# Optimization experiments

Hardware: AMD Instinct MI355X
Metric: run time of the kernel (lower is better)

## Reference

```python
import jax, jax.numpy as jnp
import numpy as np

BETA = 0.25  # commitment_beta


def _mlp(x, Ws, bs):
    # hidden layers with ReLU, final linear layer without activation
    h = x
    for W, b in zip(Ws[:-1], bs[:-1]):
        h = jax.nn.relu(h @ W + b)
    return h @ Ws[-1] + bs[-1]


def _vq(r, cb):
    # r: [B, D], cb: [K, D]
    # squared L2 distances via expansion: ||r||^2 - 2 r.cb^T + ||cb||^2
    d = (jnp.sum(r * r, axis=1, keepdims=True)
         - 2.0 * (r @ cb.T)
         + jnp.sum(cb * cb, axis=1))  # [B, K]
    idx = jnp.argmin(d, axis=1)  # [B]
    e = cb[idx]  # [B, D]
    sg = jax.lax.stop_gradient
    # per-sample codebook + commitment loss
    loss = (jnp.mean((sg(r) - e) ** 2, axis=1)
            + BETA * jnp.mean((r - sg(e)) ** 2, axis=1))  # [B]
    # straight-through estimator
    z_q = r + sg(e - r)
    return z_q, loss, idx


def setup_inputs() -> dict:
    key = jax.random.key(0)
    ks = jax.random.split(key, 16)
    B, D_IN, H1, H2, D_LAT, K = 16384, 2048, 1024, 512, 256, 1024

    def lin(k, fan_in, fan_out):
        s = 1.0 / np.sqrt(fan_in)
        return jax.random.uniform(k, (fan_in, fan_out), jnp.float32, -s, s)

    return {
        "x": jax.random.normal(ks[0], (B, D_IN), jnp.float32),
        "enc_W1": lin(ks[1], D_IN, H1), "enc_b1": jnp.zeros((H1,), jnp.float32),
        "enc_W2": lin(ks[2], H1, H2), "enc_b2": jnp.zeros((H2,), jnp.float32),
        "enc_W3": lin(ks[3], H2, D_LAT), "enc_b3": jnp.zeros((D_LAT,), jnp.float32),
        "ln_g": jnp.ones((D_LAT,), jnp.float32),
        "ln_b": jnp.zeros((D_LAT,), jnp.float32),
        "cb0": jax.random.normal(ks[4], (K, D_LAT), jnp.float32) * 0.02,
        "cb1": jax.random.normal(ks[5], (K, D_LAT), jnp.float32) * 0.02,
        "cb2": jax.random.normal(ks[6], (K, D_LAT), jnp.float32) * 0.02,
        "dec_W1": lin(ks[7], D_LAT, H2), "dec_b1": jnp.zeros((H2,), jnp.float32),
        "dec_W2": lin(ks[8], H2, H1), "dec_b2": jnp.zeros((H1,), jnp.float32),
        "dec_W3": lin(ks[9], H1, D_IN), "dec_b3": jnp.zeros((D_IN,), jnp.float32),
    }


def reference(x, enc_W1, enc_b1, enc_W2, enc_b2, enc_W3, enc_b3,
              ln_g, ln_b, cb0, cb1, cb2,
              dec_W1, dec_b1, dec_W2, dec_b2, dec_W3, dec_b3):
    z = _mlp(x, [enc_W1, enc_W2, enc_W3], [enc_b1, enc_b2, enc_b3])
    # LayerNorm over latent dim
    mu = jnp.mean(z, axis=-1, keepdims=True)
    var = jnp.var(z, axis=-1, keepdims=True)
    z = (z - mu) * jax.lax.rsqrt(var + 1e-5) * ln_g + ln_b

    sg = jax.lax.stop_gradient
    residual = z
    z_q_total = jnp.zeros_like(z)
    losses, indices = [], []
    for cb in (cb0, cb1, cb2):
        z_q, vloss, idx = _vq(residual, cb)
        residual = residual - sg(z_q)
        z_q_total = z_q_total + z_q
        losses.append(vloss)
        indices.append(idx)

    x_hat = _mlp(z_q_total, [dec_W1, dec_W2, dec_W3], [dec_b1, dec_b2, dec_b3])
    recon_loss = jnp.mean((x_hat - x) ** 2, axis=1)  # [B]
    loss = jnp.sum(jnp.stack(losses, axis=1), axis=1) + recon_loss  # [B]
    idx_out = jnp.stack(indices, axis=1)  # [B, 3]
    return x_hat, loss, idx_out
```

## Files before the change

kernel.cpp:

```cpp
#include <hip/hip_runtime.h>
#include <stdint.h>

typedef __bf16 bf16x8 __attribute__((ext_vector_type(8)));
typedef _Float16 f16x8 __attribute__((ext_vector_type(8)));
typedef float f32x4 __attribute__((ext_vector_type(4)));

#define BETA 0.25f

__device__ __forceinline__ unsigned short f2bf(float f) {
    __bf16 h = (__bf16)f;
    return __builtin_bit_cast(unsigned short, h);
}

__device__ __forceinline__ unsigned short f2h(float f) {
    _Float16 h = (_Float16)f;
    return __builtin_bit_cast(unsigned short, h);
}

__device__ __forceinline__ void split8(const float* a, uint4& vh, uint4& vl) {
    unsigned h[8], l[8];
#pragma unroll
    for (int j = 0; j < 8; ++j) {
        _Float16 hi = (_Float16)a[j];
        float hf = (float)hi;
        _Float16 lo = (_Float16)((a[j] - hf) * 2048.0f);
        h[j] = (unsigned)__builtin_bit_cast(unsigned short, hi);
        l[j] = (unsigned)__builtin_bit_cast(unsigned short, lo);
    }
    vh.x = h[0] | (h[1] << 16); vh.y = h[2] | (h[3] << 16);
    vh.z = h[4] | (h[5] << 16); vh.w = h[6] | (h[7] << 16);
    vl.x = l[0] | (l[1] << 16); vl.y = l[2] | (l[3] << 16);
    vl.z = l[4] | (l[5] << 16); vl.w = l[6] | (l[7] << 16);
}

__global__ __launch_bounds__(256) void wsplit_t(
    const float* __restrict__ W, unsigned short* __restrict__ WTh,
    unsigned short* __restrict__ WTl, int K, int N)
{
    __shared__ float tile[32][33];
    const int t = threadIdx.x;
    const int n0 = blockIdx.x * 32, k0 = blockIdx.y * 32;
    const int rr = t >> 3, c4 = (t & 7) * 4;
    float4 w = *(const float4*)(W + (size_t)(k0 + rr) * N + n0 + c4);
    tile[rr][c4 + 0] = w.x; tile[rr][c4 + 1] = w.y;
    tile[rr][c4 + 2] = w.z; tile[rr][c4 + 3] = w.w;
    __syncthreads();
    float v[4] = {tile[c4 + 0][rr], tile[c4 + 1][rr],
                  tile[c4 + 2][rr], tile[c4 + 3][rr]};
    unsigned short hh[4], ll[4];
#pragma unroll
    for (int j = 0; j < 4; ++j) {
        float s = v[j] * 32.0f;
        _Float16 hi = (_Float16)s;
        float hf = (float)hi;
        hh[j] = __builtin_bit_cast(unsigned short, hi);
        ll[j] = f2h((s - hf) * 2048.0f);
    }
    ushort4 oh, ol;
    oh.x = hh[0]; oh.y = hh[1]; oh.z = hh[2]; oh.w = hh[3];
    ol.x = ll[0]; ol.y = ll[1]; ol.z = ll[2]; ol.w = ll[3];
    *(ushort4*)(WTh + (size_t)(n0 + rr) * K + k0 + c4) = oh;
    *(ushort4*)(WTl + (size_t)(n0 + rr) * K + k0 + c4) = ol;
}

template <bool AF32, bool RELU, bool OUTSPLIT>
__global__ __launch_bounds__(256, 2) void gemm_f16x2(
    const float* __restrict__ Af,
    const unsigned short* __restrict__ Ah, const unsigned short* __restrict__ Al,
    const unsigned short* __restrict__ WTh, const unsigned short* __restrict__ WTl,
    const float* __restrict__ bias,
    void* __restrict__ Oh, unsigned short* __restrict__ Ol,
    int M, int N, int K)
{
    __shared__ unsigned short Ash[2][128][36];
    __shared__ unsigned short Asl[2][128][36];
    __shared__ unsigned short Bsh[2][128][36];
    __shared__ unsigned short Bsl[2][128][36];

    const int t = threadIdx.x;
    const int m0 = blockIdx.y * 128, n0 = blockIdx.x * 128;
    const int wave = t >> 6, lane = t & 63;
    const int wm = wave & 1, wn = wave >> 1;
    const int l15 = lane & 15, kq = lane >> 4;

    f32x4 ach[4][4] = {};
    f32x4 acl[4][4] = {};

    const int sr = t >> 1, skc = (t & 1) * 16;

    float af[16];
    uint4 vah, vah2, val, val2;
    uint4 vbh, vbh2, vbl, vbl2;

    auto LOAD = [&](int kb) {
        if (AF32) {
            const float* ap = Af + (size_t)(m0 + sr) * K + kb + skc;
            *(float4*)&af[0]  = *(const float4*)(ap);
            *(float4*)&af[4]  = *(const float4*)(ap + 4);
            *(float4*)&af[8]  = *(const float4*)(ap + 8);
            *(float4*)&af[12] = *(const float4*)(ap + 12);
        } else {
            const unsigned short* aph = Ah + (size_t)(m0 + sr) * K + kb + skc;
            const unsigned short* apl = Al + (size_t)(m0 + sr) * K + kb + skc;
            vah  = *(const uint4*)(aph);
            vah2 = *(const uint4*)(aph + 8);
            val  = *(const uint4*)(apl);
            val2 = *(const uint4*)(apl + 8);
        }
        const unsigned short* bph = WTh + (size_t)(n0 + sr) * K + kb + skc;
        const unsigned short* bpl = WTl + (size_t)(n0 + sr) * K + kb + skc;
        vbh  = *(const uint4*)(bph);
        vbh2 = *(const uint4*)(bph + 8);
        vbl  = *(const uint4*)(bpl);
        vbl2 = *(const uint4*)(bpl + 8);
    };

    auto STORE = [&](int buf) {
        uint4 wah, wah2, wal, wal2;
        if (AF32) {
            split8(&af[0], wah, wal);
            split8(&af[8], wah2, wal2);
        } else {
            wah = vah; wah2 = vah2; wal = val; wal2 = val2;
        }
        *(uint4*)&Ash[buf][sr][skc]     = wah;
        *(uint4*)&Ash[buf][sr][skc + 8] = wah2;
        *(uint4*)&Asl[buf][sr][skc]     = wal;
        *(uint4*)&Asl[buf][sr][skc + 8] = wal2;
        *(uint4*)&Bsh[buf][sr][skc]     = vbh;
        *(uint4*)&Bsh[buf][sr][skc + 8] = vbh2;
        *(uint4*)&Bsl[buf][sr][skc]     = vbl;
        *(uint4*)&Bsl[buf][sr][skc + 8] = vbl2;
    };

    const int nt = K >> 5;
    LOAD(0);
    STORE(0);
    int cur = 0;
    for (int ti = 0; ti < nt; ++ti) {
        __syncthreads();
        if (ti + 1 < nt) LOAD((ti + 1) << 5);

        f16x8 bh[4], bl[4];
#pragma unroll
        for (int bn = 0; bn < 4; ++bn) {
            bh[bn] = *(const f16x8*)&Bsh[cur][wn * 64 + bn * 16 + l15][kq * 8];
            bl[bn] = *(const f16x8*)&Bsl[cur][wn * 64 + bn * 16 + l15][kq * 8];
        }
#pragma unroll
        for (int am = 0; am < 4; ++am) {
            f16x8 ah_ = *(const f16x8*)&Ash[cur][wm * 64 + am * 16 + l15][kq * 8];
            f16x8 al_ = *(const f16x8*)&Asl[cur][wm * 64 + am * 16 + l15][kq * 8];
#pragma unroll
            for (int bn = 0; bn < 4; ++bn) {
                ach[am][bn] = __builtin_amdgcn_mfma_f32_16x16x32_f16(ah_, bh[bn], ach[am][bn], 0, 0, 0);
                acl[am][bn] = __builtin_amdgcn_mfma_f32_16x16x32_f16(ah_, bl[bn], acl[am][bn], 0, 0, 0);
                acl[am][bn] = __builtin_amdgcn_mfma_f32_16x16x32_f16(al_, bh[bn], acl[am][bn], 0, 0, 0);
            }
        }
        if (ti + 1 < nt) STORE(cur ^ 1);
        cur ^= 1;
    }

#pragma unroll
    for (int am = 0; am < 4; ++am)
#pragma unroll
        for (int bn = 0; bn < 4; ++bn)
#pragma unroll
            for (int r = 0; r < 4; ++r) {
                int row = m0 + wm * 64 + am * 16 + kq * 4 + r;
                int col = n0 + wn * 64 + bn * 16 + l15;
                float v = (ach[am][bn][r] + acl[am][bn][r] * (1.0f / 2048.0f))
                          * (1.0f / 32.0f) + bias[col];
                if (RELU) v = fmaxf(v, 0.0f);
                if (OUTSPLIT) {
                    _Float16 hi = (_Float16)v;
                    float hf = (float)hi;
                    ((unsigned short*)Oh)[(size_t)row * N + col] =
                        __builtin_bit_cast(unsigned short, hi);
                    Ol[(size_t)row * N + col] = f2h((v - hf) * 2048.0f);
                } else {
                    ((float*)Oh)[(size_t)row * N + col] = v;
                }
            }
}

template <bool RELU, bool OUTF32>
__global__ __launch_bounds__(256) void gemm_bt128(
    const unsigned short* __restrict__ A, const unsigned short* __restrict__ WT,
    const float* __restrict__ bias, void* __restrict__ Ov,
    int M, int N, int K)
{
    __shared__ unsigned short As[2][128][36];
    __shared__ unsigned short Bs[2][128][36];

    const int t = threadIdx.x;
    const int m0 = blockIdx.y * 128, n0 = blockIdx.x * 128;
    const int wave = t >> 6, lane = t & 63;
    const int wm = wave & 1, wn = wave >> 1;
    const int l15 = lane & 15, kq = lane >> 4;

    f32x4 acc[4][4] = {};

    const int sr = t >> 1, skc = (t & 1) * 16;

    uint4 va, va2, vb, vb2;
    auto LOAD = [&](int kb) {
        const unsigned short* ap = A + (size_t)(m0 + sr) * K + kb + skc;
        const unsigned short* bp = WT + (size_t)(n0 + sr) * K + kb + skc;
        va  = *(const uint4*)(ap);
        va2 = *(const uint4*)(ap + 8);
        vb  = *(const uint4*)(bp);
        vb2 = *(const uint4*)(bp + 8);
    };
    auto STORE = [&](int buf) {
        *(uint4*)&As[buf][sr][skc]     = va;
        *(uint4*)&As[buf][sr][skc + 8] = va2;
        *(uint4*)&Bs[buf][sr][skc]     = vb;
        *(uint4*)&Bs[buf][sr][skc + 8] = vb2;
    };

    const int nt = K >> 5;
    LOAD(0);
    STORE(0);
    int cur = 0;
    for (int ti = 0; ti < nt; ++ti) {
        __syncthreads();
        if (ti + 1 < nt) LOAD((ti + 1) << 5);

        bf16x8 bfr[4];
#pragma unroll
        for (int bn = 0; bn < 4; ++bn)
            bfr[bn] = *(const bf16x8*)&Bs[cur][wn * 64 + bn * 16 + l15][kq * 8];
#pragma unroll
        for (int am = 0; am < 4; ++am) {
            bf16x8 af = *(const bf16x8*)&As[cur][wm * 64 + am * 16 + l15][kq * 8];
#pragma unroll
            for (int bn = 0; bn < 4; ++bn)
                acc[am][bn] = __builtin_amdgcn_mfma_f32_16x16x32_bf16(af, bfr[bn], acc[am][bn], 0, 0, 0);
        }
        if (ti + 1 < nt) STORE(cur ^ 1);
        cur ^= 1;
    }

#pragma unroll
    for (int am = 0; am < 4; ++am)
#pragma unroll
        for (int bn = 0; bn < 4; ++bn)
#pragma unroll
            for (int r = 0; r < 4; ++r) {
                int row = m0 + wm * 64 + am * 16 + kq * 4 + r;
                int col = n0 + wn * 64 + bn * 16 + l15;
                float v = acc[am][bn][r] + bias[col];
                if (RELU) v = fmaxf(v, 0.0f);
                if (OUTF32)
                    ((float*)Ov)[(size_t)row * N + col] = v;
                else
                    ((unsigned short*)Ov)[(size_t)row * N + col] = f2bf(v);
            }
}

__global__ __launch_bounds__(256) void wtrans(
    const float* __restrict__ W, unsigned short* __restrict__ WT, int K, int N)
{
    __shared__ unsigned short tile[32][33];
    const int t = threadIdx.x;
    const int n0 = blockIdx.x * 32, k0 = blockIdx.y * 32;
    const int r = t >> 3, c4 = (t & 7) * 4;
    float4 w = *(const float4*)(W + (size_t)(k0 + r) * N + n0 + c4);
    tile[r][c4 + 0] = f2bf(w.x);
    tile[r][c4 + 1] = f2bf(w.y);
    tile[r][c4 + 2] = f2bf(w.z);
    tile[r][c4 + 3] = f2bf(w.w);
    __syncthreads();
    ushort4 o;
    o.x = tile[c4 + 0][r]; o.y = tile[c4 + 1][r];
    o.z = tile[c4 + 2][r]; o.w = tile[c4 + 3][r];
    *(ushort4*)(WT + (size_t)(n0 + r) * K + k0 + c4) = o;
}

__global__ __launch_bounds__(256) void ln_kernel(
    const float* __restrict__ Z, const float* __restrict__ g,
    const float* __restrict__ b, float* __restrict__ R)
{
    int row = blockIdx.x * 4 + (threadIdx.x >> 6);
    int lane = threadIdx.x & 63;
    float4 v = *(const float4*)(Z + (size_t)row * 256 + lane * 4);
    float s = v.x + v.y + v.z + v.w;
#pragma unroll
    for (int o = 32; o; o >>= 1) s += __shfl_xor(s, o);
    float mu = s * (1.0f / 256.0f);
    float4 d = {v.x - mu, v.y - mu, v.z - mu, v.w - mu};
    float q = d.x * d.x + d.y * d.y + d.z * d.z + d.w * d.w;
#pragma unroll
    for (int o = 32; o; o >>= 1) q += __shfl_xor(q, o);
    float var = q * (1.0f / 256.0f);
    float rs = 1.0f / sqrtf(var + 1e-5f);
    int c0 = lane * 4;
    float4 gg = *(const float4*)(g + c0);
    float4 bb = *(const float4*)(b + c0);
    float4 o4;
    o4.x = d.x * rs * gg.x + bb.x;
    o4.y = d.y * rs * gg.y + bb.y;
    o4.z = d.z * rs * gg.z + bb.z;
    o4.w = d.w * rs * gg.w + bb.w;
    *(float4*)(R + (size_t)row * 256 + c0) = o4;
}

__global__ __launch_bounds__(256) void cninit3(
    const float* __restrict__ CB0, const float* __restrict__ CB1,
    const float* __restrict__ CB2, float* __restrict__ cn,
    unsigned long long* __restrict__ amin)
{
    int b = blockIdx.x;
    int s = b >> 6, lb = b & 63;
    int g = lb * 256 + threadIdx.x;
    amin[(size_t)s * 16384 + g] = 0xFFFFFFFFFFFFFFFFULL;
    if (g < 1024) {
        const float* CB = (s == 0) ? CB0 : (s == 1) ? CB1 : CB2;
        const float* p = CB + (size_t)g * 256;
        float sum = 0.f;
        for (int d = 0; d < 256; ++d) sum = fmaf(p[d], p[d], sum);
        cn[s * 1024 + g] = sum;
    }
}

__global__ __launch_bounds__(256) void rn_kernel(
    const float* __restrict__ R, float* __restrict__ rn)
{
    __shared__ float rs[16][260];
    const int t = threadIdx.x, r0 = blockIdx.x * 16;
    {
        int row = t >> 4, j = t & 15;
#pragma unroll
        for (int q = 0; q < 4; ++q) {
            int col = j * 16 + q * 4;
            *(float4*)&rs[row][col] = *(const float4*)(R + (size_t)(r0 + row) * 256 + col);
        }
    }
    __syncthreads();
    if (t < 16) {
        float s = 0.f;
        for (int d = 0; d < 256; ++d) s = fmaf(rs[t][d], rs[t][d], s);
        rn[r0 + t] = s;
    }
}

__global__ __launch_bounds__(256) void vq_dist(
    const float* __restrict__ Rbuf, const float* __restrict__ CB,
    const float* __restrict__ rn, const float* __restrict__ cn,
    unsigned long long* __restrict__ amin)
{
    __shared__ char smem[33792];
    float (*As)[16][132] = (float (*)[16][132])smem;
    float (*Bs)[16][132] = (float (*)[16][132])(smem + 16896);
    unsigned long long (*red)[17] = (unsigned long long (*)[17])smem;

    const int t = threadIdx.x;
    const int m0 = blockIdx.y * 128, n0 = blockIdx.x * 128;
    const int tx = t & 15, ty = t >> 4;
    float c[8][8] = {};

    const int sr = t >> 1, skc = (t & 1) * 8;

    float4 a0, a1, b0, b1;
    auto LOAD = [&](int kb) {
        const float* ap = Rbuf + (size_t)(m0 + sr) * 256 + kb + skc;
        a0 = *(const float4*)(ap);
        a1 = *(const float4*)(ap + 4);
        const float* bp = CB + (size_t)(n0 + sr) * 256 + kb + skc;
        b0 = *(const float4*)(bp);
        b1 = *(const float4*)(bp + 4);
    };
    auto STORE = [&](int buf) {
        As[buf][skc + 0][sr] = a0.x; As[buf][skc + 1][sr] = a0.y;
        As[buf][skc + 2][sr] = a0.z; As[buf][skc + 3][sr] = a0.w;
        As[buf][skc + 4][sr] = a1.x; As[buf][skc + 5][sr] = a1.y;
        As[buf][skc + 6][sr] = a1.z; As[buf][skc + 7][sr] = a1.w;
        Bs[buf][skc + 0][sr] = b0.x; Bs[buf][skc + 1][sr] = b0.y;
        Bs[buf][skc + 2][sr] = b0.z; Bs[buf][skc + 3][sr] = b0.w;
        Bs[buf][skc + 4][sr] = b1.x; Bs[buf][skc + 5][sr] = b1.y;
        Bs[buf][skc + 6][sr] = b1.z; Bs[buf][skc + 7][sr] = b1.w;
    };

    LOAD(0);
    STORE(0);
    int cur = 0;
    for (int ti = 0; ti < 16; ++ti) {
        __syncthreads();
        if (ti + 1 < 16) LOAD((ti + 1) * 16);

#pragma unroll
        for (int k = 0; k < 16; ++k) {
            float a[8], b[8];
            *(float4*)&a[0] = *(const float4*)&As[cur][k][ty * 8];
            *(float4*)&a[4] = *(const float4*)&As[cur][k][ty * 8 + 4];
            *(float4*)&b[0] = *(const float4*)&Bs[cur][k][tx * 4];
            *(float4*)&b[4] = *(const float4*)&Bs[cur][k][64 + tx * 4];
#pragma unroll
            for (int i = 0; i < 8; ++i)
#pragma unroll
                for (int j = 0; j < 8; ++j)
                    c[i][j] = fmaf(a[i], b[j], c[i][j]);
        }
        if (ti + 1 < 16) STORE(cur ^ 1);
        cur ^= 1;
    }

    float rnv[8], cnv[8];
    *(float4*)&rnv[0] = *(const float4*)(rn + m0 + ty * 8);
    *(float4*)&rnv[4] = *(const float4*)(rn + m0 + ty * 8 + 4);
    *(float4*)&cnv[0] = *(const float4*)(cn + n0 + tx * 4);
    *(float4*)&cnv[4] = *(const float4*)(cn + n0 + 64 + tx * 4);

    __syncthreads();

#pragma unroll
    for (int i = 0; i < 8; ++i) {
        unsigned long long best = 0xFFFFFFFFFFFFFFFFULL;
#pragma unroll
        for (int j = 0; j < 8; ++j) {
            float dist = (rnv[i] - 2.0f * c[i][j]) + cnv[j];
            int col = n0 + (j < 4 ? tx * 4 + j : 64 + tx * 4 + (j - 4));
            unsigned long long p =
                ((unsigned long long)__builtin_bit_cast(unsigned int, dist) << 32) |
                (unsigned int)col;
            if (p < best) best = p;
        }
        red[ty * 8 + i][tx] = best;
    }
    __syncthreads();
    if (t < 128) {
        unsigned long long b = red[t][0];
#pragma unroll
        for (int j = 1; j < 16; ++j) {
            unsigned long long v = red[t][j];
            if (v < b) b = v;
        }
        atomicMin(amin + m0 + t, b);
    }
}

__global__ __launch_bounds__(256) void vq_update(
    float* __restrict__ Rbuf, float* __restrict__ ZQ, float* __restrict__ lossf,
    const float* __restrict__ CB, const unsigned long long* __restrict__ amin,
    float* __restrict__ idx_out, unsigned short* __restrict__ ZQB, int stage)
{
    __shared__ float lred[16][17];
    const int t = threadIdx.x, r0 = blockIdx.x * 16;
    const int row = r0 + (t >> 4), c16 = (t & 15) * 16;
    unsigned int idx = (unsigned int)(amin[row] & 0xffffffffu);
    const float* e = CB + (size_t)idx * 256 + c16;
    float* rp = Rbuf + (size_t)row * 256 + c16;
    float* zp = ZQ + (size_t)row * 256 + c16;
    float part = 0.f;
#pragma unroll
    for (int q = 0; q < 4; ++q) {
        float4 ev = *(const float4*)(e + q * 4);
        float4 rv = *(const float4*)(rp + q * 4);
        float4 dv = {rv.x - ev.x, rv.y - ev.y, rv.z - ev.z, rv.w - ev.w};
        *(float4*)(rp + q * 4) = dv;
        if (stage == 0) {
            *(float4*)(zp + q * 4) = ev;
        } else if (stage == 1) {
            float4 zv = *(const float4*)(zp + q * 4);
            zv.x += ev.x; zv.y += ev.y; zv.z += ev.z; zv.w += ev.w;
            *(float4*)(zp + q * 4) = zv;
        } else {
            float4 zv = *(const float4*)(zp + q * 4);
            zv.x += ev.x; zv.y += ev.y; zv.z += ev.z; zv.w += ev.w;
            ushort4 zb;
            zb.x = f2bf(zv.x); zb.y = f2bf(zv.y);
            zb.z = f2bf(zv.z); zb.w = f2bf(zv.w);
            *(ushort4*)(ZQB + (size_t)row * 256 + c16 + q * 4) = zb;
        }
        part = fmaf(dv.x, dv.x, part);
        part = fmaf(dv.y, dv.y, part);
        part = fmaf(dv.z, dv.z, part);
        part = fmaf(dv.w, dv.w, part);
    }
    lred[t >> 4][t & 15] = part;
    __syncthreads();
    if (t < 16) {
        float s = 0.f;
        for (int j = 0; j < 16; ++j) s += lred[t][j];
        float m = s * (1.0f / 256.0f);
        float l = m + BETA * m;
        int gr = r0 + t;
        if (stage == 0) lossf[gr] = l;
        else            lossf[gr] += l;
        idx_out[(size_t)gr * 3 + stage] =
            (float)(unsigned int)(amin[gr] & 0xffffffffu);
    }
}

__global__ __launch_bounds__(256) void recon_kernel(
    const float* __restrict__ XH, const float* __restrict__ X,
    const float* __restrict__ LOSS_IN, float* __restrict__ LOSS_OUT)
{
    __shared__ float wsum[4];
    int row = blockIdx.x, t = threadIdx.x;
    float4 h0 = *(const float4*)(XH + (size_t)row * 2048 + t * 8);
    float4 h1 = *(const float4*)(XH + (size_t)row * 2048 + t * 8 + 4);
    float4 x0 = *(const float4*)(X + (size_t)row * 2048 + t * 8);
    float4 x1 = *(const float4*)(X + (size_t)row * 2048 + t * 8 + 4);
    float h[8] = {h0.x, h0.y, h0.z, h0.w, h1.x, h1.y, h1.z, h1.w};
    float xv[8] = {x0.x, x0.y, x0.z, x0.w, x1.x, x1.y, x1.z, x1.w};
    float s = 0.f;
#pragma unroll
    for (int j = 0; j < 8; ++j) {
        float d = h[j] - xv[j];
        s = fmaf(d, d, s);
    }
#pragma unroll
    for (int o = 32; o; o >>= 1) s += __shfl_xor(s, o);
    if ((t & 63) == 0) wsum[t >> 6] = s;
    __syncthreads();
    if (t == 0) {
        float tot = wsum[0] + wsum[1] + wsum[2] + wsum[3];
        LOSS_OUT[row] = LOSS_IN[row] + tot * (1.0f / 2048.0f);
    }
}

extern "C" void kernel_launch(void* const* d_in, const int* in_sizes, int n_in,
                              void* d_out, int out_size, void* d_ws, size_t ws_size,
                              hipStream_t stream)
{
    const float* x      = (const float*)d_in[0];
    const float* enc_W1 = (const float*)d_in[1];
    const float* enc_b1 = (const float*)d_in[2];
    const float* enc_W2 = (const float*)d_in[3];
    const float* enc_b2 = (const float*)d_in[4];
    const float* enc_W3 = (const float*)d_in[5];
    const float* enc_b3 = (const float*)d_in[6];
    const float* ln_g   = (const float*)d_in[7];
    const float* ln_b   = (const float*)d_in[8];
    const float* cb0    = (const float*)d_in[9];
    const float* cb1    = (const float*)d_in[10];
    const float* cb2    = (const float*)d_in[11];
    const float* dec_W1 = (const float*)d_in[12];
    const float* dec_b1 = (const float*)d_in[13];
    const float* dec_W2 = (const float*)d_in[14];
    const float* dec_b2 = (const float*)d_in[15];
    const float* dec_W3 = (const float*)d_in[16];
    const float* dec_b3 = (const float*)d_in[17];

    const int B = 16384, D_IN = 2048, H1 = 1024, H2 = 512, D_LAT = 256;

    char* ws = (char*)d_ws;
    unsigned short* h1h = (unsigned short*)(ws);
    unsigned short* h1l = (unsigned short*)(ws + (32u << 20));
    unsigned short* h2h = (unsigned short*)(ws + (64u << 20));
    unsigned short* h2l = (unsigned short*)(ws + (80u << 20));
    float* z     = (float*)(ws + (96u << 20));
    float* r     = (float*)(ws + (112u << 20));
    float* zq    = (float*)(ws + (96u << 20));
    unsigned short* w1th = (unsigned short*)(ws + (96u << 20));
    unsigned short* w1tl = (unsigned short*)(ws + (100u << 20));
    unsigned short* w2th = (unsigned short*)(ws + (104u << 20));
    unsigned short* w2tl = (unsigned short*)(ws + (105u << 20));
    unsigned short* w3th = (unsigned short*)(ws + (112u << 20));
    unsigned short* w3tl = (unsigned short*)(ws + (113u << 20));
    unsigned short* d1  = (unsigned short*)(ws);
    unsigned short* d2  = (unsigned short*)(ws + (16u << 20));
    unsigned short* wt3 = (unsigned short*)(ws + (48u << 20));
    unsigned short* wt2 = (unsigned short*)(ws + (52u << 20));
    float* lossf = (float*)(ws + (64u << 20));
    float* cn3   = (float*)(ws + (65u << 20));
    unsigned long long* amin3 = (unsigned long long*)(ws + (66u << 20));
    float* rnb   = (float*)(ws + (67u << 20));
    unsigned short* zqb = (unsigned short*)(ws + (68u << 20));
    unsigned short* wt1 = (unsigned short*)(ws + (76u << 20));

    float* xhat     = (float*)d_out;
    float* loss_out = xhat + (size_t)B * D_IN;
    float* idx_out  = loss_out + B;

    wsplit_t<<<dim3(H1 / 32, D_IN / 32), 256, 0, stream>>>(enc_W1, w1th, w1tl, D_IN, H1);
    wsplit_t<<<dim3(H2 / 32, H1 / 32), 256, 0, stream>>>(enc_W2, w2th, w2tl, H1, H2);
    wsplit_t<<<dim3(D_LAT / 32, H2 / 32), 256, 0, stream>>>(enc_W3, w3th, w3tl, H2, D_LAT);

    gemm_f16x2<true, true, true><<<dim3(H1 / 128, B / 128), 256, 0, stream>>>(
        x, nullptr, nullptr, w1th, w1tl, enc_b1, h1h, h1l, B, H1, D_IN);
    gemm_f16x2<false, true, true><<<dim3(H2 / 128, B / 128), 256, 0, stream>>>(
        nullptr, h1h, h1l, w2th, w2tl, enc_b2, h2h, h2l, B, H2, H1);
    wtrans<<<dim3(H1 / 32, H2 / 32), 256, 0, stream>>>(dec_W2, wt2, H2, H1);
    wtrans<<<dim3(D_IN / 32, H1 / 32), 256, 0, stream>>>(dec_W3, wt3, H1, D_IN);
    gemm_f16x2<false, false, false><<<dim3(D_LAT / 128, B / 128), 256, 0, stream>>>(
        nullptr, h2h, h2l, w3th, w3tl, enc_b3, z, nullptr, B, D_LAT, H2);
    ln_kernel<<<B / 4, 256, 0, stream>>>(z, ln_g, ln_b, r);

    cninit3<<<192, 256, 0, stream>>>(cb0, cb1, cb2, cn3, amin3);
    wtrans<<<dim3(H2 / 32, D_LAT / 32), 256, 0, stream>>>(dec_W1, wt1, D_LAT, H2);

    const float* cbs[3] = {cb0, cb1, cb2};
    for (int s = 0; s < 3; ++s) {
        rn_kernel<<<B / 16, 256, 0, stream>>>(r, rnb);
        vq_dist<<<dim3(1024 / 128, B / 128), 256, 0, stream>>>(
            r, cbs[s], rnb, cn3 + s * 1024, amin3 + (size_t)s * 16384);
        vq_update<<<B / 16, 256, 0, stream>>>(
            r, zq, lossf, cbs[s], amin3 + (size_t)s * 16384, idx_out, zqb, s);
    }

    gemm_bt128<true, false><<<dim3(H2 / 128, B / 128), 256, 0, stream>>>(
        zqb, wt1, dec_b1, d1, B, H2, D_LAT);
    gemm_bt128<true, false><<<dim3(H1 / 128, B / 128), 256, 0, stream>>>(
        d1, wt2, dec_b2, d2, B, H1, H2);
    gemm_bt128<false, true><<<dim3(D_IN / 128, B / 128), 256, 0, stream>>>(
        d2, wt3, dec_b3, xhat, B, D_IN, H1);
    recon_kernel<<<B, 256, 0, stream>>>(xhat, x, lossf, loss_out);
}
```

Measured before the change: 1.330 ms.

## Replace double-buffered LDS pipeline in vq_dist with single-buffer two-barrier loop

The codebook distance GEMM kernel drops its register-prefetch double buffering and goes back to one LDS buffer, with two barriers per k-tile. The reduction scratch becomes its own shared array instead of aliasing the tile buffers. This lowers register pressure and may raise occupancy, but global loads are no longer overlapped with the FMA work of the previous tile. Shared memory use goes up because the reduction array is now separate.

```diff
diff --git a/kernel.cpp b/kernel.cpp
--- a/kernel.cpp
+++ b/kernel.cpp
@@ -351,10 +351,9 @@
     const float* __restrict__ rn, const float* __restrict__ cn,
     unsigned long long* __restrict__ amin)
 {
-    __shared__ char smem[33792];
-    float (*As)[16][132] = (float (*)[16][132])smem;
-    float (*Bs)[16][132] = (float (*)[16][132])(smem + 16896);
-    unsigned long long (*red)[17] = (unsigned long long (*)[17])smem;
+    __shared__ float As[16][132];
+    __shared__ float Bs[16][132];
+    __shared__ unsigned long long red[128][17];
 
     const int t = threadIdx.x;
     const int m0 = blockIdx.y * 128, n0 = blockIdx.x * 128;
@@ -363,48 +362,38 @@
 
     const int sr = t >> 1, skc = (t & 1) * 8;
 
-    float4 a0, a1, b0, b1;
-    auto LOAD = [&](int kb) {
+    for (int kb = 0; kb < 256; kb += 16) {
         const float* ap = Rbuf + (size_t)(m0 + sr) * 256 + kb + skc;
-        a0 = *(const float4*)(ap);
-        a1 = *(const float4*)(ap + 4);
+        float4 a0 = *(const float4*)(ap);
+        float4 a1 = *(const float4*)(ap + 4);
         const float* bp = CB + (size_t)(n0 + sr) * 256 + kb + skc;
-        b0 = *(const float4*)(bp);
-        b1 = *(const float4*)(bp + 4);
-    };
-    auto STORE = [&](int buf) {
-        As[buf][skc + 0][sr] = a0.x; As[buf][skc + 1][sr] = a0.y;
-        As[buf][skc + 2][sr] = a0.z; As[buf][skc + 3][sr] = a0.w;
-        As[buf][skc + 4][sr] = a1.x; As[buf][skc + 5][sr] = a1.y;
-        As[buf][skc + 6][sr] = a1.z; As[buf][skc + 7][sr] = a1.w;
-        Bs[buf][skc + 0][sr] = b0.x; Bs[buf][skc + 1][sr] = b0.y;
-        Bs[buf][skc + 2][sr] = b0.z; Bs[buf][skc + 3][sr] = b0.w;
-        Bs[buf][skc + 4][sr] = b1.x; Bs[buf][skc + 5][sr] = b1.y;
-        Bs[buf][skc + 6][sr] = b1.z; Bs[buf][skc + 7][sr] = b1.w;
-    };
-
-    LOAD(0);
-    STORE(0);
-    int cur = 0;
-    for (int ti = 0; ti < 16; ++ti) {
+        float4 b0 = *(const float4*)(bp);
+        float4 b1 = *(const float4*)(bp + 4);
+
         __syncthreads();
-        if (ti + 1 < 16) LOAD((ti + 1) * 16);
+        As[skc + 0][sr] = a0.x; As[skc + 1][sr] = a0.y;
+        As[skc + 2][sr] = a0.z; As[skc + 3][sr] = a0.w;
+        As[skc + 4][sr] = a1.x; As[skc + 5][sr] = a1.y;
+        As[skc + 6][sr] = a1.z; As[skc + 7][sr] = a1.w;
+        Bs[skc + 0][sr] = b0.x; Bs[skc + 1][sr] = b0.y;
+        Bs[skc + 2][sr] = b0.z; Bs[skc + 3][sr] = b0.w;
+        Bs[skc + 4][sr] = b1.x; Bs[skc + 5][sr] = b1.y;
+        Bs[skc + 6][sr] = b1.z; Bs[skc + 7][sr] = b1.w;
+        __syncthreads();
 
 #pragma unroll
         for (int k = 0; k < 16; ++k) {
             float a[8], b[8];
-            *(float4*)&a[0] = *(const float4*)&As[cur][k][ty * 8];
-            *(float4*)&a[4] = *(const float4*)&As[cur][k][ty * 8 + 4];
-            *(float4*)&b[0] = *(const float4*)&Bs[cur][k][tx * 4];
-            *(float4*)&b[4] = *(const float4*)&Bs[cur][k][64 + tx * 4];
+            *(float4*)&a[0] = *(const float4*)&As[k][ty * 8];
+            *(float4*)&a[4] = *(const float4*)&As[k][ty * 8 + 4];
+            *(float4*)&b[0] = *(const float4*)&Bs[k][tx * 4];
+            *(float4*)&b[4] = *(const float4*)&Bs[k][64 + tx * 4];
 #pragma unroll
             for (int i = 0; i < 8; ++i)
 #pragma unroll
                 for (int j = 0; j < 8; ++j)
                     c[i][j] = fmaf(a[i], b[j], c[i][j]);
         }
-        if (ti + 1 < 16) STORE(cur ^ 1);
-        cur ^= 1;
     }
 
     float rnv[8], cnv[8];
@@ -412,8 +401,6 @@
     *(float4*)&rnv[4] = *(const float4*)(rn + m0 + ty * 8 + 4);
     *(float4*)&cnv[0] = *(const float4*)(cn + n0 + tx * 4);
     *(float4*)&cnv[4] = *(const float4*)(cn + n0 + 64 + tx * 4);
-
-    __syncthreads();
 
 #pragma unroll
     for (int i = 0; i < 8; ++i) {
```

New measurement: 1.167 ms. 12.2% less time.
